# Performance work log

Measured on AMD Instinct MI355X. Metric: run time of the kernel, lower is better.

The kernel has to match this reference:

```python
import jax, jax.numpy as jnp
import numpy as np

K = 3          # kernel_size
G = 16         # group_number
BN_EPS = 1e-3  # keras BatchNormalization default epsilon


def setup_inputs() -> dict:
    key = jax.random.key(0)
    ks = jax.random.split(key, 4)
    B, H, W, C = 8, 64, 64, 256
    R = 4  # reduction_ratio
    return {
        "x": jax.random.normal(ks[0], (B, H, W, C), dtype=jnp.float32),
        "W1": jax.random.normal(ks[1], (C, C // R), dtype=jnp.float32) * 0.05,
        "b1": jnp.zeros((C // R,), dtype=jnp.float32),
        "gamma": jnp.ones((C // R,), dtype=jnp.float32),
        "beta": jnp.zeros((C // R,), dtype=jnp.float32),
        "mov_mean": jnp.zeros((C // R,), dtype=jnp.float32),
        "mov_var": jnp.ones((C // R,), dtype=jnp.float32),
        "W2": jax.random.normal(ks[2], (C // R, K * K * G), dtype=jnp.float32) * 0.05,
        "b2": jnp.zeros((K * K * G,), dtype=jnp.float32),
    }


def reference(x, W1, b1, gamma, beta, mov_mean, mov_var, W2, b2):
    B, H, W, C = x.shape
    # kernel generation: 1x1 conv -> BN (inference) -> ReLU -> 1x1 conv
    h = jnp.einsum("bhwc,cd->bhwd", x, W1) + b1
    h = (h - mov_mean) * (gamma / jnp.sqrt(mov_var + BN_EPS)) + beta
    h = jax.nn.relu(h)
    kernel = jnp.einsum("bhwd,de->bhwe", h, W2) + b2      # (B,H,W,K*K*G)
    kernel = kernel.reshape(B, H, W, K * K, 1, G)
    # extract_patches (SAME, stride 1): tf orders last axis as (ki,kj,channel)
    p = K // 2
    xp = jnp.pad(x, ((0, 0), (p, p), (p, p), (0, 0)))
    patches = jnp.stack(
        [xp[:, i:i + H, j:j + W, :] for i in range(K) for j in range(K)],
        axis=3,
    )  # (B,H,W,K*K,C)
    patches = patches.reshape(B, H, W, K * K, C // G, G)
    out = jnp.sum(kernel * patches, axis=3)               # (B,H,W,C//G,G)
    out = out.reshape(B, H, W, C)
    return out, kernel
```

## Files before the change

### kernel.cpp

```cpp
#include <hip/hip_runtime.h>
#include <hip/hip_bf16.h>

typedef __attribute__((ext_vector_type(8))) short bf16x8;
typedef __attribute__((ext_vector_type(4))) float f32x4;

#define NPIX 32768

__device__ __forceinline__ ushort f2bf(float f) {
    __hip_bfloat16 h = __float2bfloat16(f);
    ushort u; __builtin_memcpy(&u, &h, 2);
    return u;
}

__global__ __launch_bounds__(1024, 1) void fused_kernel(
        const float* __restrict__ x,
        const float* __restrict__ W1, const float* __restrict__ b1,
        const float* __restrict__ gamma, const float* __restrict__ beta,
        const float* __restrict__ mean, const float* __restrict__ var,
        const float* __restrict__ W2, const float* __restrict__ b2,
        float* __restrict__ ker, float* __restrict__ out) {
    __shared__ __align__(16) char smem[133120];
    const int t = threadIdx.x;
    const int wv = t >> 6, ln = t & 63;
    char* arena = smem + wv * 5120;
    char* w1s   = smem + 81920;
    char* w2s   = smem + 114688;
    const int bid = (int)blockIdx.x;
    const int img = bid & 7;
    const int rp  = bid >> 3;
    const int i   = rp * 2 + (wv >> 3);
    const int lb  = img * 64 + i;
    const int j0  = (wv & 7) * 8;
    const int pw  = lb * 64 + j0;
    const int r16 = ln & 15, g = ln >> 4;
    const int q8  = r16 & 7;

    #pragma unroll
    for (int m = 0; m < 2; m++) {
        int idx = m * 1024 + t;
        int ln2 = idx & 63, dt = (idx >> 6) & 3, kk = idx >> 8;
        int d = dt * 16 + (ln2 & 15);
        float sc = gamma[d] * rsqrtf(var[d] + 1e-3f);
        int cbase = kk * 32 + (ln2 >> 4) * 8;
        ushort tmp[8];
        #pragma unroll
        for (int cc = 0; cc < 8; cc++)
            tmp[cc] = f2bf(W1[(cbase + cc) * 64 + d] * sc);
        __builtin_memcpy(w1s + idx * 16, tmp, 16);
    }
    #pragma unroll
    for (int m = 0; m < 2; m++) {
        int idx = m * 1024 + t;
        if (idx < 1152) {
            int ln2 = idx & 63, rem = idx >> 6;
            int et = rem % 9, kk = rem / 9;
            int e = et * 16 + (ln2 & 15);
            int dbase = kk * 32 + (ln2 >> 4) * 8;
            ushort tmp[8];
            #pragma unroll
            for (int cc = 0; cc < 8; cc++)
                tmp[cc] = f2bf(W2[(dbase + cc) * 144 + e]);
            __builtin_memcpy(w2s + idx * 16, tmp, 16);
        }
    }
    float b1fv[4];
    #pragma unroll
    for (int dt = 0; dt < 4; dt++) {
        int d = dt * 16 + r16;
        float sc = gamma[d] * rsqrtf(var[d] + 1e-3f);
        b1fv[dt] = (b1[d] - mean[d]) * sc + beta[d];
    }

    {
        const float4* xg = (const float4*)(x + (size_t)pw * 256);
        #pragma unroll
        for (int it = 0; it < 8; it++) {
            float4 v = xg[it * 64 + ln];
            ushort4 b4; b4.x = f2bf(v.x); b4.y = f2bf(v.y);
            b4.z = f2bf(v.z); b4.w = f2bf(v.w);
            int bcol = (ln * 8) ^ (it << 4);
            *(ushort4*)(arena + it * 512 + bcol) = b4;
        }
    }
    __syncthreads();

    f32x4 acc[4];
    #pragma unroll
    for (int dt = 0; dt < 4; dt++) {
        float bv = b1fv[dt];
        acc[dt] = (f32x4){bv, bv, bv, bv};
    }
    #pragma unroll
    for (int kk = 0; kk < 8; kk++) {
        int bcA = (kk * 64 + g * 16) ^ (q8 << 4);
        bf16x8 av = *(const bf16x8*)(arena + q8 * 512 + bcA);
        #pragma unroll
        for (int dt = 0; dt < 4; dt++) {
            bf16x8 bv = *(const bf16x8*)(w1s + (((kk * 4 + dt) << 6) + ln) * 16);
            acc[dt] = __builtin_amdgcn_mfma_f32_16x16x32_bf16(av, bv, acc[dt], 0, 0, 0);
        }
    }

    #pragma unroll
    for (int dt = 0; dt < 4; dt++) {
        #pragma unroll
        for (int r = 0; r < 4; r++) {
            int q = g * 4 + r;
            if (q < 8) {
                int bcol = ((dt * 16 + r16) * 2) ^ (q << 4);
                *(ushort*)(arena + 4096 + q * 128 + bcol) = f2bf(fmaxf(acc[dt][r], 0.f));
            }
        }
    }

    const f32x4* xv4 = (const f32x4*)x;
    const f32x4 z4 = {0.f, 0.f, 0.f, 0.f};
    f32x4 wa[3], wb[3], wc[3], wd[3];
    #pragma unroll
    for (int r = 0; r < 3; r++) {
        int row = i + r - 1;
        bool rv = (unsigned)row < 64u;
        const size_t rb = (size_t)(lb + r - 1) * 64;
        wa[r] = (rv && j0 > 0) ? xv4[(rb + (j0 - 1)) * 64 + ln] : z4;
        wb[r] = rv ? xv4[(rb + j0) * 64 + ln] : z4;
        wc[r] = rv ? xv4[(rb + j0 + 1) * 64 + ln] : z4;
        wd[r] = rv ? xv4[(rb + j0 + 2) * 64 + ln] : z4;
    }

    f32x4 acc2[9];
    #pragma unroll
    for (int et = 0; et < 9; et++) {
        float bv = b2[et * 16 + r16];
        acc2[et] = (f32x4){bv, bv, bv, bv};
    }
    #pragma unroll
    for (int kk = 0; kk < 2; kk++) {
        int bcA = (kk * 64 + g * 16) ^ (q8 << 4);
        bf16x8 av = *(const bf16x8*)(arena + 4096 + q8 * 128 + bcA);
        #pragma unroll
        for (int et = 0; et < 9; et++) {
            bf16x8 bv = *(const bf16x8*)(w2s + (((kk * 9 + et) << 6) + ln) * 16);
            acc2[et] = __builtin_amdgcn_mfma_f32_16x16x32_bf16(av, bv, acc2[et], 0, 0, 0);
        }
    }

    float* ksf = (float*)arena;
    #pragma unroll
    for (int et = 0; et < 9; et++) {
        #pragma unroll
        for (int r = 0; r < 4; r++) {
            int q = g * 4 + r;
            if (q < 8)
                ksf[q * 148 + et * 16 + r16] = acc2[et][r];
        }
    }

    const int s4 = (ln & 3) * 4;
    #pragma unroll
    for (int pp = 0; pp < 8; pp++) {
        const int j = j0 + pp;
        const float* kp = ksf + pp * 148 + s4;
        f32x4 o = {0.f, 0.f, 0.f, 0.f};
        #pragma unroll
        for (int r = 0; r < 3; r++) {
            o += (*(const f32x4*)(kp + (r * 3 + 0) * 16)) * wa[r];
            o += (*(const f32x4*)(kp + (r * 3 + 1) * 16)) * wb[r];
            o += (*(const f32x4*)(kp + (r * 3 + 2) * 16)) * wc[r];
        }
        __builtin_nontemporal_store(o, &((f32x4*)out)[(size_t)(lb * 64 + j) * 64 + ln]);
        #pragma unroll
        for (int r = 0; r < 3; r++) { wa[r] = wb[r]; wb[r] = wc[r]; wc[r] = wd[r]; }
        if (pp < 6) {
            const int jn = j + 3;
            const bool cv = jn < 64;
            #pragma unroll
            for (int r = 0; r < 3; r++) {
                int row = i + r - 1;
                bool rv = (unsigned)row < 64u;
                wd[r] = (rv && cv)
                    ? xv4[((size_t)(lb + r - 1) * 64 + jn) * 64 + ln] : z4;
            }
        }
    }

    {
        float* kerW = ker + (size_t)pw * 144;
        #pragma unroll
        for (int m = 0; m < 5; m++) {
            int fidx = m * 64 + ln;
            if (fidx < 288) {
                int row  = fidx / 36;
                int col4 = fidx - row * 36;
                f32x4 v = *(const f32x4*)(ksf + row * 148 + col4 * 4);
                __builtin_nontemporal_store(v, (f32x4*)(kerW + fidx * 4));
            }
        }
    }
}

extern "C" void kernel_launch(void* const* d_in, const int* in_sizes, int n_in,
                              void* d_out, int out_size, void* d_ws, size_t ws_size,
                              hipStream_t stream) {
    const float* x     = (const float*)d_in[0];
    const float* W1    = (const float*)d_in[1];
    const float* b1    = (const float*)d_in[2];
    const float* gamma = (const float*)d_in[3];
    const float* beta  = (const float*)d_in[4];
    const float* mmean = (const float*)d_in[5];
    const float* mvar  = (const float*)d_in[6];
    const float* W2    = (const float*)d_in[7];
    const float* b2    = (const float*)d_in[8];

    float* out_main = (float*)d_out;
    float* out_ker  = (float*)d_out + 8388608;

    fused_kernel<<<NPIX / 128, 1024, 0, stream>>>(
        x, W1, b1, gamma, beta, mmean, mvar, W2, b2, out_ker, out_main);
}
```

Measured before the change: 22.35 us.

## Pair waves to fill 16-row MFMA tiles and split output columns between them

```diff
diff --git a/kernel.cpp b/kernel.cpp
--- a/kernel.cpp
+++ b/kernel.cpp
@@ -19,21 +19,22 @@
         const float* __restrict__ mean, const float* __restrict__ var,
         const float* __restrict__ W2, const float* __restrict__ b2,
         float* __restrict__ ker, float* __restrict__ out) {
-    __shared__ __align__(16) char smem[133120];
+    __shared__ __align__(16) char smem[145408];
     const int t = threadIdx.x;
     const int wv = t >> 6, ln = t & 63;
-    char* arena = smem + wv * 5120;
-    char* w1s   = smem + 81920;
-    char* w2s   = smem + 114688;
+    const int pair = wv >> 1, sub = wv & 1;
+    char* arena = smem + pair * 11776;
+    char* w1s   = smem + 94208;
+    char* w2s   = smem + 126976;
     const int bid = (int)blockIdx.x;
     const int img = bid & 7;
     const int rp  = bid >> 3;
-    const int i   = rp * 2 + (wv >> 3);
+    const int i   = rp * 2 + (pair >> 2);
     const int lb  = img * 64 + i;
-    const int j0  = (wv & 7) * 8;
-    const int pw  = lb * 64 + j0;
+    const int j0p = (pair & 3) * 16;
+    const int pwp = lb * 64 + j0p;
+    const int j0  = j0p + sub * 8;
     const int r16 = ln & 15, g = ln >> 4;
-    const int q8  = r16 & 7;
 
     #pragma unroll
     for (int m = 0; m < 2; m++) {
@@ -48,9 +49,8 @@
             tmp[cc] = f2bf(W1[(cbase + cc) * 64 + d] * sc);
         __builtin_memcpy(w1s + idx * 16, tmp, 16);
     }
-    #pragma unroll
-    for (int m = 0; m < 2; m++) {
-        int idx = m * 1024 + t;
+    {
+        int idx = t;
         if (idx < 1152) {
             int ln2 = idx & 63, rem = idx >> 6;
             int et = rem % 9, kk = rem / 9;
@@ -62,54 +62,67 @@
                 tmp[cc] = f2bf(W2[(dbase + cc) * 144 + e]);
             __builtin_memcpy(w2s + idx * 16, tmp, 16);
         }
-    }
-    float b1fv[4];
-    #pragma unroll
-    for (int dt = 0; dt < 4; dt++) {
-        int d = dt * 16 + r16;
+        idx = 1024 + t;
+        if (idx < 1152) {
+            int ln2 = idx & 63, rem = idx >> 6;
+            int et = rem % 9, kk = rem / 9;
+            int e = et * 16 + (ln2 & 15);
+            int dbase = kk * 32 + (ln2 >> 4) * 8;
+            ushort tmp[8];
+            #pragma unroll
+            for (int cc = 0; cc < 8; cc++)
+                tmp[cc] = f2bf(W2[(dbase + cc) * 144 + e]);
+            __builtin_memcpy(w2s + idx * 16, tmp, 16);
+        }
+    }
+    float b1fv[2];
+    #pragma unroll
+    for (int dtl = 0; dtl < 2; dtl++) {
+        int d = (sub * 2 + dtl) * 16 + r16;
         float sc = gamma[d] * rsqrtf(var[d] + 1e-3f);
-        b1fv[dt] = (b1[d] - mean[d]) * sc + beta[d];
+        b1fv[dtl] = (b1[d] - mean[d]) * sc + beta[d];
     }
 
     {
-        const float4* xg = (const float4*)(x + (size_t)pw * 256);
+        const float4* xg = (const float4*)(x + (size_t)(pwp + sub * 8) * 256);
         #pragma unroll
         for (int it = 0; it < 8; it++) {
+            int row = sub * 8 + it;
             float4 v = xg[it * 64 + ln];
             ushort4 b4; b4.x = f2bf(v.x); b4.y = f2bf(v.y);
             b4.z = f2bf(v.z); b4.w = f2bf(v.w);
-            int bcol = (ln * 8) ^ (it << 4);
-            *(ushort4*)(arena + it * 512 + bcol) = b4;
+            int bcol = (ln * 8) ^ ((it & 7) << 4);
+            *(ushort4*)(arena + 2048 + row * 512 + bcol) = b4;
         }
     }
     __syncthreads();
 
-    f32x4 acc[4];
-    #pragma unroll
-    for (int dt = 0; dt < 4; dt++) {
-        float bv = b1fv[dt];
-        acc[dt] = (f32x4){bv, bv, bv, bv};
+    f32x4 acc[2];
+    #pragma unroll
+    for (int dtl = 0; dtl < 2; dtl++) {
+        float bv = b1fv[dtl];
+        acc[dtl] = (f32x4){bv, bv, bv, bv};
     }
     #pragma unroll
     for (int kk = 0; kk < 8; kk++) {
-        int bcA = (kk * 64 + g * 16) ^ (q8 << 4);
-        bf16x8 av = *(const bf16x8*)(arena + q8 * 512 + bcA);
-        #pragma unroll
-        for (int dt = 0; dt < 4; dt++) {
+        int bcA = (kk * 64 + g * 16) ^ ((r16 & 7) << 4);
+        bf16x8 av = *(const bf16x8*)(arena + 2048 + r16 * 512 + bcA);
+        #pragma unroll
+        for (int dtl = 0; dtl < 2; dtl++) {
+            int dt = sub * 2 + dtl;
             bf16x8 bv = *(const bf16x8*)(w1s + (((kk * 4 + dt) << 6) + ln) * 16);
-            acc[dt] = __builtin_amdgcn_mfma_f32_16x16x32_bf16(av, bv, acc[dt], 0, 0, 0);
-        }
-    }
-
-    #pragma unroll
-    for (int dt = 0; dt < 4; dt++) {
+            acc[dtl] = __builtin_amdgcn_mfma_f32_16x16x32_bf16(av, bv, acc[dtl], 0, 0, 0);
+        }
+    }
+
+    #pragma unroll
+    for (int dtl = 0; dtl < 2; dtl++) {
+        int dt = sub * 2 + dtl;
         #pragma unroll
         for (int r = 0; r < 4; r++) {
             int q = g * 4 + r;
-            if (q < 8) {
-                int bcol = ((dt * 16 + r16) * 2) ^ (q << 4);
-                *(ushort*)(arena + 4096 + q * 128 + bcol) = f2bf(fmaxf(acc[dt][r], 0.f));
-            }
+            int bcol = ((dt * 16 + r16) * 2) ^ ((q & 7) << 4);
+            *(ushort*)(arena + q * 128 + bcol) = f2bf(fmaxf(acc[dtl][r], 0.f));
         }
     }
 
@@ -127,39 +140,68 @@
         wd[r] = rv ? xv4[(rb + j0 + 2) * 64 + ln] : z4;
     }
 
-    f32x4 acc2[9];
-    #pragma unroll
-    for (int et = 0; et < 9; et++) {
-        float bv = b2[et * 16 + r16];
-        acc2[et] = (f32x4){bv, bv, bv, bv};
-    }
-    #pragma unroll
-    for (int kk = 0; kk < 2; kk++) {
-        int bcA = (kk * 64 + g * 16) ^ (q8 << 4);
-        bf16x8 av = *(const bf16x8*)(arena + 4096 + q8 * 128 + bcA);
-        #pragma unroll
-        for (int et = 0; et < 9; et++) {
-            bf16x8 bv = *(const bf16x8*)(w2s + (((kk * 9 + et) << 6) + ln) * 16);
-            acc2[et] = __builtin_amdgcn_mfma_f32_16x16x32_bf16(av, bv, acc2[et], 0, 0, 0);
-        }
-    }
-
-    float* ksf = (float*)arena;
-    #pragma unroll
-    for (int et = 0; et < 9; et++) {
-        #pragma unroll
-        for (int r = 0; r < 4; r++) {
-            int q = g * 4 + r;
-            if (q < 8)
-                ksf[q * 148 + et * 16 + r16] = acc2[et][r];
-        }
-    }
+    __syncthreads();
+
+    float* ksf = (float*)(arena + 2048);
+    if (sub == 0) {
+        f32x4 acc2[5];
+        #pragma unroll
+        for (int etl = 0; etl < 5; etl++) {
+            float bv = b2[etl * 16 + r16];
+            acc2[etl] = (f32x4){bv, bv, bv, bv};
+        }
+        #pragma unroll
+        for (int kk = 0; kk < 2; kk++) {
+            int bcA = (kk * 64 + g * 16) ^ ((r16 & 7) << 4);
+            bf16x8 av = *(const bf16x8*)(arena + r16 * 128 + bcA);
+            #pragma unroll
+            for (int etl = 0; etl < 5; etl++) {
+                bf16x8 bv = *(const bf16x8*)(w2s + (((kk * 9 + etl) << 6) + ln) * 16);
+                acc2[etl] = __builtin_amdgcn_mfma_f32_16x16x32_bf16(av, bv, acc2[etl], 0, 0, 0);
+            }
+        }
+        #pragma unroll
+        for (int etl = 0; etl < 5; etl++) {
+            #pragma unroll
+            for (int r = 0; r < 4; r++) {
+                int q = g * 4 + r;
+                ksf[q * 148 + etl * 16 + r16] = acc2[etl][r];
+            }
+        }
+    } else {
+        f32x4 acc2[4];
+        #pragma unroll
+        for (int etl = 0; etl < 4; etl++) {
+            float bv = b2[(5 + etl) * 16 + r16];
+            acc2[etl] = (f32x4){bv, bv, bv, bv};
+        }
+        #pragma unroll
+        for (int kk = 0; kk < 2; kk++) {
+            int bcA = (kk * 64 + g * 16) ^ ((r16 & 7) << 4);
+            bf16x8 av = *(const bf16x8*)(arena + r16 * 128 + bcA);
+            #pragma unroll
+            for (int etl = 0; etl < 4; etl++) {
+                bf16x8 bv = *(const bf16x8*)(w2s + (((kk * 9 + 5 + etl) << 6) + ln) * 16);
+                acc2[etl] = __builtin_amdgcn_mfma_f32_16x16x32_bf16(av, bv, acc2[etl], 0, 0, 0);
+            }
+        }
+        #pragma unroll
+        for (int etl = 0; etl < 4; etl++) {
+            #pragma unroll
+            for (int r = 0; r < 4; r++) {
+                int q = g * 4 + r;
+                ksf[q * 148 + (5 + etl) * 16 + r16] = acc2[etl][r];
+            }
+        }
+    }
+
+    __syncthreads();
 
     const int s4 = (ln & 3) * 4;
     #pragma unroll
     for (int pp = 0; pp < 8; pp++) {
         const int j = j0 + pp;
-        const float* kp = ksf + pp * 148 + s4;
+        const float* kp = ksf + (sub * 8 + pp) * 148 + s4;
         f32x4 o = {0.f, 0.f, 0.f, 0.f};
         #pragma unroll
         for (int r = 0; r < 3; r++) {
@@ -184,14 +226,14 @@
     }
 
     {
-        float* kerW = ker + (size_t)pw * 144;
+        float* kerW = ker + (size_t)(pwp + sub * 8) * 144;
         #pragma unroll
         for (int m = 0; m < 5; m++) {
             int fidx = m * 64 + ln;
             if (fidx < 288) {
                 int row  = fidx / 36;
                 int col4 = fidx - row * 36;
-                f32x4 v = *(const f32x4*)(ksf + row * 148 + col4 * 4);
+                f32x4 v = *(const f32x4*)(ksf + (sub * 8 + row) * 148 + col4 * 4);
                 __builtin_nontemporal_store(v, (f32x4*)(kerW + fidx * 4));
             }
         }
```

Measured after the change: 22.00 us. No clear change (-1.6%).
